# Kernel optimization log

Hardware: AMD Instinct MI355X
Metric: run time of the kernel (lower is better)

Reference implementation:

```python
import jax, jax.numpy as jnp
import numpy as np

N, T = 4096, 128
D, R = 8, 32
ENC_H, NADE_H, K_MIX = 64, 64, 10


def setup_inputs() -> dict:
    key = jax.random.key(0)
    ks = jax.random.split(key, 17)
    s = 0.1
    rn = lambda k, shp, sc: (sc * jax.random.normal(k, shp)).astype(jnp.float32)
    return {
        "x": rn(ks[0], (N, 1, T), 1.0),
        "enc1_w": rn(ks[1], (1, ENC_H), s),
        "enc1_b": rn(ks[2], (ENC_H,), s),
        "enc2_w": rn(ks[3], (ENC_H, D), s),
        "enc2_b": rn(ks[4], (D,), s),
        "A": rn(ks[5], (R, D, R), s),
        "init_w": rn(ks[6], (1, R), s),
        "nade1_w": rn(ks[7], (R, NADE_H), s),
        "nade1_b": rn(ks[8], (NADE_H,), s),
        "nade2_w": rn(ks[9], (NADE_H, NADE_H), s),
        "nade2_b": rn(ks[10], (NADE_H,), s),
        "mu_w": rn(ks[11], (NADE_H, K_MIX), s),
        "mu_b": rn(ks[12], (K_MIX,), s),
        "sig_w": rn(ks[13], (NADE_H, K_MIX), s),
        "sig_b": rn(ks[14], (K_MIX,), s),
        "alpha_w": rn(ks[15], (NADE_H, K_MIX), s),
        "alpha_b": rn(ks[16], (K_MIX,), s),
    }


def reference(x, enc1_w, enc1_b, enc2_w, enc2_b, A, init_w,
              nade1_w, nade1_b, nade2_w, nade2_b,
              mu_w, mu_b, sig_w, sig_b, alpha_w, alpha_b):
    LOG2PI = jnp.log(2.0 * jnp.pi).astype(x.dtype)

    def phi(x_t, h):
        # x_t: [N], h: [N, R] -> mixture-of-Gaussians log prob [N]
        h = jnp.tanh(h)
        h = jax.nn.relu(h @ nade1_w + nade1_b)
        h = jax.nn.relu(h @ nade2_w + nade2_b)
        mu = h @ mu_w + mu_b                       # [N, K]
        log_sig = h @ sig_w + sig_b                # sig = exp(log_sig)
        log_alpha = jax.nn.log_softmax(h @ alpha_w + alpha_b, axis=1)
        z = (x_t[:, None] - mu) * jnp.exp(-log_sig)
        comp_lp = -0.5 * z * z - log_sig - 0.5 * LOG2PI
        return jax.scipy.special.logsumexp(log_alpha + comp_lp, axis=1)

    xt = x[:, 0, :]                                # [N, T]
    # vectorized encoder over all timesteps: tanh(relu(x*W1+b1)@W2+b2) -> [N, T, D]
    e = jax.nn.relu(xt[:, :, None] * enc1_w[0] + enc1_b)
    enc = jnp.tanh(e @ enc2_w + enc2_b)

    h0 = jnp.broadcast_to(init_w, (xt.shape[0], R))
    res0 = phi(xt[:, 0], h0)

    def step(carry, inputs):
        tmp, res = carry
        e_prev, x_cur = inputs                     # [N, D], [N]
        tmp = jnp.einsum('nd,ni,idj->nj', e_prev, tmp, A)
        res = res + phi(x_cur, tmp)
        return (tmp, res), None

    xs = (jnp.moveaxis(enc[:, :-1, :], 1, 0),      # [T-1, N, D]
          jnp.moveaxis(xt[:, 1:], 1, 0))           # [T-1, N]
    (_, res), _ = jax.lax.scan(step, (h0, res0), xs)
    return jnp.exp(res)
```

## Files before the change

### kernel.cpp

```cpp
#include <hip/hip_runtime.h>

#define DEV __device__ __forceinline__

typedef __attribute__((ext_vector_type(8))) short short8v;
typedef __attribute__((ext_vector_type(4))) float f32x4;

DEV unsigned short bfr(float f) {
    unsigned u = __float_as_uint(f);
    return (unsigned short)((u + 0x7fffu + ((u >> 16) & 1u)) >> 16);
}
DEV short bft(float f) { return (short)(__float_as_uint(f) >> 16); }
DEV float bf2f(unsigned short h) { return __uint_as_float(((unsigned)h) << 16); }
DEV float frcp(float x) { return __builtin_amdgcn_rcpf(x); }
DEV float ftanh(float x) { float e = __expf(2.0f * x); return 1.0f - 2.0f * frcp(e + 1.0f); }

constexpr int NN = 4096, TT = 128;
#define MFMA32(a, b, c) __builtin_amdgcn_mfma_f32_16x16x32_bf16(a, b, c, 0, 0, 0)


__global__ __launch_bounds__(512) __attribute__((amdgpu_waves_per_eu(2)))
void wfa_kernel(
    const float* __restrict__ x,
    const float* __restrict__ e1w, const float* __restrict__ e1b,
    const float* __restrict__ e2w, const float* __restrict__ e2b,
    const float* __restrict__ A,
    const float* __restrict__ initw,
    const float* __restrict__ n1w, const float* __restrict__ n1b,
    const float* __restrict__ n2w, const float* __restrict__ n2b,
    const float* __restrict__ muw, const float* __restrict__ mub,
    const float* __restrict__ sgw, const float* __restrict__ sgb,
    const float* __restrict__ alw, const float* __restrict__ alb,
    float* __restrict__ out)
{
    __shared__ __align__(16) unsigned short enc_l[TT * 128];
    __shared__ __align__(16) float x_l[16 * 130];
    __shared__ __align__(16) short8v ring_l[2][8][64];
    __shared__ __align__(16) float n1b_l[64], n2b_l[64], hb_l[48];
    __shared__ float part_l[8][16];

    const int tid = threadIdx.x;
    const int wv = tid >> 6, lane = tid & 63;
    const int quad = lane >> 4, col = lane & 15;
    const int n0 = blockIdx.x * 16;
    const f32x4 z4 = {0.f, 0.f, 0.f, 0.f};

    for (int i = tid; i < 16 * TT; i += 512)
        x_l[(i >> 7) * 130 + (i & 127)] = x[(n0 + (i >> 7)) * TT + (i & 127)];
    if (tid < 64) { n1b_l[tid] = n1b[tid]; n2b_l[tid] = n2b[tid]; }
    if (tid >= 64 && tid < 112) {
        const int i = tid - 64, mt = i >> 4, k = i & 15;
        hb_l[i] = (k < 10) ? ((mt == 0) ? mub[k] : (mt == 1) ? sgb[k] : alb[k]) : 0.f;
    }

    __syncthreads();

    {
        float e1c[16], e1bc[16];
        #pragma unroll
        for (int kc = 0; kc < 2; ++kc)
            #pragma unroll
            for (int jj = 0; jj < 8; ++jj) {
                const int f = kc * 32 + (jj >> 2) * 16 + quad * 4 + (jj & 3);
                e1c[kc * 8 + jj] = e1w[f];
                e1bc[kc * 8 + jj] = e1b[f];
            }
        short8v E2A[2];
        #pragma unroll
        for (int kc = 0; kc < 2; ++kc)
            #pragma unroll
            for (int jj = 0; jj < 8; ++jj)
                E2A[kc][jj] = (short)(col < 8
                    ? bfr(e2w[(kc * 32 + (jj >> 2) * 16 + quad * 4 + (jj & 3)) * 8 + col]) : 0);
        float e2bc[4];
        #pragma unroll
        for (int r = 0; r < 4; ++r) e2bc[r] = (quad < 2) ? e2b[quad * 4 + r] : 0.f;

        const int tbase = wv * 16;
        #pragma unroll 1
        for (int nn = 0; nn < 16; ++nn) {
            const float xs = x_l[nn * 130 + tbase + col];
            short8v eB[2];
            #pragma unroll
            for (int kc = 0; kc < 2; ++kc)
                #pragma unroll
                for (int jj = 0; jj < 8; ++jj)
                    eB[kc][jj] = bft(fmaxf(fmaf(xs, e1c[kc * 8 + jj], e1bc[kc * 8 + jj]), 0.f));
            f32x4 d = MFMA32(E2A[0], eB[0], z4);
            d = MFMA32(E2A[1], eB[1], d);
            if (quad < 2) {
                #pragma unroll
                for (int r = 0; r < 4; ++r)
                    enc_l[(tbase + col) * 128 + nn * 8 + quad * 4 + r] = bfr(ftanh(d[r] + e2bc[r]));
            }
        }
    }
    __syncthreads();

    if (wv == 0) {
        short8v A2f[16];
        #pragma unroll
        for (int mt = 0; mt < 16; ++mt)
            #pragma unroll
            for (int jj = 0; jj < 8; ++jj)
                A2f[mt][jj] = (short)bfr(
                    A[((jj >> 2) * 16 + quad * 4 + (jj & 3)) * 256 + (mt >> 1) * 32 + (mt & 1) * 16 + col]);

        short8v tmpB;
        #pragma unroll
        for (int jj = 0; jj < 8; ++jj)
            tmpB[jj] = (short)bfr(initw[(jj >> 2) * 16 + quad * 4 + (jj & 3)]);

        asm volatile("s_setprio 2");

        short8v e8c = *(const short8v*)&enc_l[0 * 128 + col * 8];

        #pragma unroll 1
        for (int b = 0; b <= 16; ++b) {
            if (b < 16) {
                #pragma unroll 1
                for (int i = 0; i < 8; ++i) {
                    const int t = b * 8 + i;
                    if (t > 0) {
                        const short8v e8n = *(const short8v*)&enc_l[t * 128 + col * 8];
                        float ev[8];
                        #pragma unroll
                        for (int d = 0; d < 8; ++d) ev[d] = bf2f((unsigned short)e8c[d]);
                        short8v nt;
                        #pragma unroll
                        for (int h = 0; h < 2; ++h) {
                            f32x4 D[8];
                            #pragma unroll
                            for (int d = 0; d < 8; ++d) D[d] = MFMA32(A2f[2 * d + h], tmpB, z4);
                            #pragma unroll
                            for (int r = 0; r < 4; ++r) {
                                float s = 0.f;
                                #pragma unroll
                                for (int d = 0; d < 8; ++d) s = fmaf(ev[d], D[d][r], s);
                                nt[h * 4 + r] = bft(s);
                            }
                        }
                        tmpB = nt;
                        e8c = e8n;
                    }
                    ring_l[b & 1][i][lane] = tmpB;
                }
            }
            __syncthreads();
        }
        if (lane < 16) part_l[0][lane] = 0.f;
    } else {
        short8v W1f[4];
        #pragma unroll
        for (int mt = 0; mt < 4; ++mt)
            #pragma unroll
            for (int jj = 0; jj < 8; ++jj)
                W1f[mt][jj] = (short)bfr(n1w[((jj >> 2) * 16 + quad * 4 + (jj & 3)) * 64 + mt * 16 + col]);
        short8v W2f[4][2];
        #pragma unroll
        for (int mt = 0; mt < 4; ++mt)
            #pragma unroll
            for (int kb = 0; kb < 2; ++kb)
                #pragma unroll
                for (int jj = 0; jj < 8; ++jj)
                    W2f[mt][kb][jj] = (short)bfr(
                        n2w[(kb * 32 + (jj >> 2) * 16 + quad * 4 + (jj & 3)) * 64 + mt * 16 + col]);
        short8v Whf[3][2];
        #pragma unroll
        for (int mt = 0; mt < 3; ++mt) {
            const float* Wh = (mt == 0) ? muw : (mt == 1) ? sgw : alw;
            #pragma unroll
            for (int kb = 0; kb < 2; ++kb)
                #pragma unroll
                for (int jj = 0; jj < 8; ++jj)
                    Whf[mt][kb][jj] = (short)(col < 10
                        ? bfr(Wh[(kb * 32 + (jj >> 2) * 16 + quad * 4 + (jj & 3)) * 10 + col]) : 0);
        }

        float res2 = 0.f;
        const float CST = 0.91893853320467274f;

        #pragma unroll 1
        for (int b = 0; b <= 16; ++b) {
            if (b >= 1) {
                #pragma unroll 1
                for (int i = wv - 1; i < 8; i += 7) {
                    const int t = (b - 1) * 8 + i;
                    const short8v tf = ring_l[(b - 1) & 1][i][lane];
                    short8v thB;
                    #pragma unroll
                    for (int jj = 0; jj < 8; ++jj)
                        thB[jj] = bft(ftanh(bf2f((unsigned short)tf[jj])));

                    short8v h1B[2];
                    #pragma unroll
                    for (int mt = 0; mt < 4; ++mt) {
                        const f32x4 c = *(const f32x4*)&n1b_l[mt * 16 + quad * 4];
                        const f32x4 d = MFMA32(W1f[mt], thB, c);
                        #pragma unroll
                        for (int r = 0; r < 4; ++r)
                            h1B[mt >> 1][(mt & 1) * 4 + r] = bft(fmaxf(d[r], 0.f));
                    }
                    short8v h2B[2];
                    #pragma unroll
                    for (int mt = 0; mt < 4; ++mt) {
                        const f32x4 c = *(const f32x4*)&n2b_l[mt * 16 + quad * 4];
                        f32x4 d = MFMA32(W2f[mt][0], h1B[0], c);
                        d = MFMA32(W2f[mt][1], h1B[1], d);
                        #pragma unroll
                        for (int r = 0; r < 4; ++r)
                            h2B[mt >> 1][(mt & 1) * 4 + r] = bft(fmaxf(d[r], 0.f));
                    }
                    f32x4 hd[3];
                    #pragma unroll
                    for (int mt = 0; mt < 3; ++mt) {
                        const f32x4 c = *(const f32x4*)&hb_l[mt * 16 + quad * 4];
                        f32x4 d = MFMA32(Whf[mt][0], h2B[0], c);
                        hd[mt] = MFMA32(Whf[mt][1], h2B[1], d);
                    }
                    const float xt = x_l[col * 130 + t];
                    float s1 = 0.f, s2 = 0.f;
                    #pragma unroll
                    for (int r = 0; r < 4; ++r) {
                        const bool valid = (quad * 4 + r) < 10;
                        const float mu = hd[0][r], sg = hd[1][r], la = hd[2][r];
                        const float e1t = __expf(la);
                        const float z = (xt - mu) * __expf(-sg);
                        const float e2t = __expf(la - sg - fmaf(0.5f * z, z, CST));
                        s1 += valid ? e1t : 0.f;
                        s2 += valid ? e2t : 0.f;
                    }
                    s1 += __shfl_xor(s1, 16, 64);  s2 += __shfl_xor(s2, 16, 64);
                    s1 += __shfl_xor(s1, 32, 64);  s2 += __shfl_xor(s2, 32, 64);
                    res2 += __log2f(s2) - __log2f(s1);
                }
            }
            __syncthreads();
        }
        if (lane < 16) part_l[wv][lane] = res2;
    }

    __syncthreads();
    if (tid < 16) {
        float s = 0.f;
        #pragma unroll
        for (int w = 0; w < 8; ++w) s += part_l[w][tid];
        out[n0 + tid] = exp2f(s);
    }
}

extern "C" void kernel_launch(void* const* d_in, const int* in_sizes, int n_in,
                              void* d_out, int out_size, void* d_ws, size_t ws_size,
                              hipStream_t stream) {
    wfa_kernel<<<dim3(NN / 16), dim3(512), 0, stream>>>(
        (const float*)d_in[0],  (const float*)d_in[1],  (const float*)d_in[2],
        (const float*)d_in[3],  (const float*)d_in[4],  (const float*)d_in[5],
        (const float*)d_in[6],  (const float*)d_in[7],  (const float*)d_in[8],
        (const float*)d_in[9],  (const float*)d_in[10], (const float*)d_in[11],
        (const float*)d_in[12], (const float*)d_in[13], (const float*)d_in[14],
        (const float*)d_in[15], (const float*)d_in[16], (float*)d_out);
}
```

Before: 142.1 us.

## Replace barrier-blocked producer/consumer with ticketed ring and 15 consumer waves

Doubles the block to 1024 threads so one producer wave runs the serial recurrence while 15 consumer waves evaluate the NADE mixture. Per-batch __syncthreads is replaced by a 16-slot LDS ring with a head counter, atomic ticket dispatch to consumers, and producer backpressure that polls the minimum consumer progress. This is meant to stop the producer stalling at block barriers and to spread the phi work across more waves. The cost is higher register pressure (waves_per_eu 4), spin-wait polling, and subtle memory-ordering assumptions in LDS.

New measurement: 163.6 us. 1.15x slower.

```diff
diff --git a/kernel.cpp b/kernel.cpp
--- a/kernel.cpp
+++ b/kernel.cpp
@@ -14,11 +14,11 @@
 DEV float frcp(float x) { return __builtin_amdgcn_rcpf(x); }
 DEV float ftanh(float x) { float e = __expf(2.0f * x); return 1.0f - 2.0f * frcp(e + 1.0f); }
 
-constexpr int NN = 4096, TT = 128;
+constexpr int NN = 4096, TT = 128, RING = 16;
 #define MFMA32(a, b, c) __builtin_amdgcn_mfma_f32_16x16x32_bf16(a, b, c, 0, 0, 0)
 
 
-__global__ __launch_bounds__(512) __attribute__((amdgpu_waves_per_eu(2)))
+__global__ __launch_bounds__(1024) __attribute__((amdgpu_waves_per_eu(4)))
 void wfa_kernel(
     const float* __restrict__ x,
     const float* __restrict__ e1w, const float* __restrict__ e1b,
@@ -34,9 +34,12 @@
 {
     __shared__ __align__(16) unsigned short enc_l[TT * 128];
     __shared__ __align__(16) float x_l[16 * 130];
-    __shared__ __align__(16) short8v ring_l[2][8][64];
+    __shared__ __align__(16) short8v ring_l[RING][64];
     __shared__ __align__(16) float n1b_l[64], n2b_l[64], hb_l[48];
-    __shared__ float part_l[8][16];
+    __shared__ float part_l[16][16];
+    __shared__ int head_l;
+    __shared__ int ticket_l;
+    __shared__ int prog_l[15];
 
     const int tid = threadIdx.x;
     const int wv = tid >> 6, lane = tid & 63;
@@ -44,13 +47,15 @@
     const int n0 = blockIdx.x * 16;
     const f32x4 z4 = {0.f, 0.f, 0.f, 0.f};
 
-    for (int i = tid; i < 16 * TT; i += 512)
+    for (int i = tid; i < 16 * TT; i += 1024)
         x_l[(i >> 7) * 130 + (i & 127)] = x[(n0 + (i >> 7)) * TT + (i & 127)];
     if (tid < 64) { n1b_l[tid] = n1b[tid]; n2b_l[tid] = n2b[tid]; }
     if (tid >= 64 && tid < 112) {
         const int i = tid - 64, mt = i >> 4, k = i & 15;
         hb_l[i] = (k < 10) ? ((mt == 0) ? mub[k] : (mt == 1) ? sgb[k] : alb[k]) : 0.f;
     }
+    if (tid >= 112 && tid < 127) prog_l[tid - 112] = 0;
+    if (tid == 127) { head_l = 0; ticket_l = 0; }
 
     __syncthreads();
 
@@ -75,9 +80,10 @@
         #pragma unroll
         for (int r = 0; r < 4; ++r) e2bc[r] = (quad < 2) ? e2b[quad * 4 + r] : 0.f;
 
-        const int tbase = wv * 16;
+        const int tbase = (wv & 7) * 16;
+        const int nlo = (wv >> 3) * 8;
         #pragma unroll 1
-        for (int nn = 0; nn < 16; ++nn) {
+        for (int nn = nlo; nn < nlo + 8; ++nn) {
             const float xs = x_l[nn * 130 + tbase + col];
             short8v eB[2];
             #pragma unroll
@@ -115,37 +121,47 @@
         short8v e8c = *(const short8v*)&enc_l[0 * 128 + col * 8];
 
         #pragma unroll 1
-        for (int b = 0; b <= 16; ++b) {
-            if (b < 16) {
-                #pragma unroll 1
-                for (int i = 0; i < 8; ++i) {
-                    const int t = b * 8 + i;
-                    if (t > 0) {
-                        const short8v e8n = *(const short8v*)&enc_l[t * 128 + col * 8];
-                        float ev[8];
+        for (int t = 0; t < TT; ++t) {
+            if (t > 0) {
+                const short8v e8n = *(const short8v*)&enc_l[t * 128 + col * 8];
+                float ev[8];
+                #pragma unroll
+                for (int d = 0; d < 8; ++d) ev[d] = bf2f((unsigned short)e8c[d]);
+                short8v nt;
+                #pragma unroll
+                for (int h = 0; h < 2; ++h) {
+                    f32x4 D[8];
+                    #pragma unroll
+                    for (int d = 0; d < 8; ++d) D[d] = MFMA32(A2f[2 * d + h], tmpB, z4);
+                    #pragma unroll
+                    for (int r = 0; r < 4; ++r) {
+                        float s = 0.f;
                         #pragma unroll
-                        for (int d = 0; d < 8; ++d) ev[d] = bf2f((unsigned short)e8c[d]);
-                        short8v nt;
-                        #pragma unroll
-                        for (int h = 0; h < 2; ++h) {
-                            f32x4 D[8];
-                            #pragma unroll
-                            for (int d = 0; d < 8; ++d) D[d] = MFMA32(A2f[2 * d + h], tmpB, z4);
-                            #pragma unroll
-                            for (int r = 0; r < 4; ++r) {
-                                float s = 0.f;
-                                #pragma unroll
-                                for (int d = 0; d < 8; ++d) s = fmaf(ev[d], D[d][r], s);
-                                nt[h * 4 + r] = bft(s);
-                            }
-                        }
-                        tmpB = nt;
-                        e8c = e8n;
+                        for (int d = 0; d < 8; ++d) s = fmaf(ev[d], D[d][r], s);
+                        nt[h * 4 + r] = bft(s);
                     }
-                    ring_l[b & 1][i][lane] = tmpB;
                 }
-            }
-            __syncthreads();
+                tmpB = nt;
+                e8c = e8n;
+            }
+            ring_l[t & (RING - 1)][lane] = tmpB;
+            if (t & 1) {
+                __threadfence_block();
+                if (lane == 0) *(volatile int*)&head_l = t + 1;
+            }
+            if ((t & 7) == 7 && t >= 15 && t < 120) {
+                const int need = t - 7;
+                while (true) {
+                    int p = (lane < 15) ? *(volatile int*)&prog_l[lane] : (1 << 30);
+                    #pragma unroll
+                    for (int s = 1; s < 64; s <<= 1) {
+                        const int q = __shfl_xor(p, s, 64);
+                        p = (q < p) ? q : p;
+                    }
+                    if (p >= need) break;
+                    __builtin_amdgcn_s_sleep(4);
+                }
+            }
         }
         if (lane < 16) part_l[0][lane] = 0.f;
     } else {
@@ -178,64 +194,71 @@
 
         float res2 = 0.f;
         const float CST = 0.91893853320467274f;
-
-        #pragma unroll 1
-        for (int b = 0; b <= 16; ++b) {
-            if (b >= 1) {
-                #pragma unroll 1
-                for (int i = wv - 1; i < 8; i += 7) {
-                    const int t = (b - 1) * 8 + i;
-                    const short8v tf = ring_l[(b - 1) & 1][i][lane];
-                    short8v thB;
-                    #pragma unroll
-                    for (int jj = 0; jj < 8; ++jj)
-                        thB[jj] = bft(ftanh(bf2f((unsigned short)tf[jj])));
-
-                    short8v h1B[2];
-                    #pragma unroll
-                    for (int mt = 0; mt < 4; ++mt) {
-                        const f32x4 c = *(const f32x4*)&n1b_l[mt * 16 + quad * 4];
-                        const f32x4 d = MFMA32(W1f[mt], thB, c);
-                        #pragma unroll
-                        for (int r = 0; r < 4; ++r)
-                            h1B[mt >> 1][(mt & 1) * 4 + r] = bft(fmaxf(d[r], 0.f));
-                    }
-                    short8v h2B[2];
-                    #pragma unroll
-                    for (int mt = 0; mt < 4; ++mt) {
-                        const f32x4 c = *(const f32x4*)&n2b_l[mt * 16 + quad * 4];
-                        f32x4 d = MFMA32(W2f[mt][0], h1B[0], c);
-                        d = MFMA32(W2f[mt][1], h1B[1], d);
-                        #pragma unroll
-                        for (int r = 0; r < 4; ++r)
-                            h2B[mt >> 1][(mt & 1) * 4 + r] = bft(fmaxf(d[r], 0.f));
-                    }
-                    f32x4 hd[3];
-                    #pragma unroll
-                    for (int mt = 0; mt < 3; ++mt) {
-                        const f32x4 c = *(const f32x4*)&hb_l[mt * 16 + quad * 4];
-                        f32x4 d = MFMA32(Whf[mt][0], h2B[0], c);
-                        hd[mt] = MFMA32(Whf[mt][1], h2B[1], d);
-                    }
-                    const float xt = x_l[col * 130 + t];
-                    float s1 = 0.f, s2 = 0.f;
-                    #pragma unroll
-                    for (int r = 0; r < 4; ++r) {
-                        const bool valid = (quad * 4 + r) < 10;
-                        const float mu = hd[0][r], sg = hd[1][r], la = hd[2][r];
-                        const float e1t = __expf(la);
-                        const float z = (xt - mu) * __expf(-sg);
-                        const float e2t = __expf(la - sg - fmaf(0.5f * z, z, CST));
-                        s1 += valid ? e1t : 0.f;
-                        s2 += valid ? e2t : 0.f;
-                    }
-                    s1 += __shfl_xor(s1, 16, 64);  s2 += __shfl_xor(s2, 16, 64);
-                    s1 += __shfl_xor(s1, 32, 64);  s2 += __shfl_xor(s2, 32, 64);
-                    res2 += __log2f(s2) - __log2f(s1);
-                }
-            }
-            __syncthreads();
-        }
+        const int c = wv - 1;
+
+        int t;
+        if (lane == 0) { t = atomicAdd(&ticket_l, 1); *(volatile int*)&prog_l[c] = t; }
+        t = __shfl(t, 0, 64);
+
+        while (t < TT) {
+            while (*(volatile int*)&head_l <= t) __builtin_amdgcn_s_sleep(1);
+            asm volatile("" ::: "memory");
+            const short8v tf = ring_l[t & (RING - 1)][lane];
+            __threadfence_block();
+            int tn;
+            if (lane == 0) { tn = atomicAdd(&ticket_l, 1); *(volatile int*)&prog_l[c] = tn; }
+            tn = __shfl(tn, 0, 64);
+
+            short8v thB;
+            #pragma unroll
+            for (int jj = 0; jj < 8; ++jj)
+                thB[jj] = bft(ftanh(bf2f((unsigned short)tf[jj])));
+
+            short8v h1B[2];
+            #pragma unroll
+            for (int mt = 0; mt < 4; ++mt) {
+                const f32x4 cc = *(const f32x4*)&n1b_l[mt * 16 + quad * 4];
+                const f32x4 d = MFMA32(W1f[mt], thB, cc);
+                #pragma unroll
+                for (int r = 0; r < 4; ++r)
+                    h1B[mt >> 1][(mt & 1) * 4 + r] = bft(fmaxf(d[r], 0.f));
+            }
+            short8v h2B[2];
+            #pragma unroll
+            for (int mt = 0; mt < 4; ++mt) {
+                const f32x4 cc = *(const f32x4*)&n2b_l[mt * 16 + quad * 4];
+                f32x4 d = MFMA32(W2f[mt][0], h1B[0], cc);
+                d = MFMA32(W2f[mt][1], h1B[1], d);
+                #pragma unroll
+                for (int r = 0; r < 4; ++r)
+                    h2B[mt >> 1][(mt & 1) * 4 + r] = bft(fmaxf(d[r], 0.f));
+            }
+            f32x4 hd[3];
+            #pragma unroll
+            for (int mt = 0; mt < 3; ++mt) {
+                const f32x4 cc = *(const f32x4*)&hb_l[mt * 16 + quad * 4];
+                f32x4 d = MFMA32(Whf[mt][0], h2B[0], cc);
+                hd[mt] = MFMA32(Whf[mt][1], h2B[1], d);
+            }
+            const float xt = x_l[col * 130 + t];
+            float s1 = 0.f, s2 = 0.f;
+            #pragma unroll
+            for (int r = 0; r < 4; ++r) {
+                const bool valid = (quad * 4 + r) < 10;
+                const float mu = hd[0][r], sg = hd[1][r], la = hd[2][r];
+                const float e1t = __expf(la);
+                const float z = (xt - mu) * __expf(-sg);
+                const float e2t = __expf(la - sg - fmaf(0.5f * z, z, CST));
+                s1 += valid ? e1t : 0.f;
+                s2 += valid ? e2t : 0.f;
+            }
+            s1 += __shfl_xor(s1, 16, 64);  s2 += __shfl_xor(s2, 16, 64);
+            s1 += __shfl_xor(s1, 32, 64);  s2 += __shfl_xor(s2, 32, 64);
+            res2 += __log2f(s2) - __log2f(s1);
+
+            t = tn;
+        }
+        if (lane == 0) *(volatile int*)&prog_l[c] = 1 << 30;
         if (lane < 16) part_l[wv][lane] = res2;
     }
 
@@ -243,7 +266,7 @@
     if (tid < 16) {
         float s = 0.f;
         #pragma unroll
-        for (int w = 0; w < 8; ++w) s += part_l[w][tid];
+        for (int w = 0; w < 16; ++w) s += part_l[w][tid];
         out[n0 + tid] = exp2f(s);
     }
 }
@@ -251,7 +274,7 @@
 extern "C" void kernel_launch(void* const* d_in, const int* in_sizes, int n_in,
                               void* d_out, int out_size, void* d_ws, size_t ws_size,
                               hipStream_t stream) {
-    wfa_kernel<<<dim3(NN / 16), dim3(512), 0, stream>>>(
+    wfa_kernel<<<dim3(NN / 16), dim3(1024), 0, stream>>>(
         (const float*)d_in[0],  (const float*)d_in[1],  (const float*)d_in[2],
         (const float*)d_in[3],  (const float*)d_in[4],  (const float*)d_in[5],
         (const float*)d_in[6],  (const float*)d_in[7],  (const float*)d_in[8],
```
